# Optimization experiments

Measured on AMD Instinct MI355X. Metric: run time of the kernel, lower is better.

Reference implementation:

```python
import jax, jax.numpy as jnp
import numpy as np

H, DK = 8, 64
INNER = H * DK  # 512


def rel_shift(x):
    # Transformer-XL relative shift (NeMo style): pad left, reshape, drop first row.
    b, h, q, p = x.shape
    x = jnp.pad(x, ((0, 0), (0, 0), (0, 0), (1, 0)))
    x = x.reshape(b, h, p + 1, q)[:, :, 1:]
    return x.reshape(b, h, q, p)


def setup_inputs() -> dict:
    key = jax.random.key(0)
    ks = jax.random.split(key, 16)
    B, T, D = 8, 1024, 512
    s_d = 1.0 / np.sqrt(D)
    s_i = 1.0 / np.sqrt(INNER)
    return {
        "x": jax.random.normal(ks[0], (B, T, D), jnp.float32),
        "pos_emb": jax.random.normal(ks[1], (1, 2 * T - 1, INNER), jnp.float32),
        "w_qkv": jax.random.normal(ks[2], (D, 3 * INNER), jnp.float32) * s_d,
        "w_q": jax.random.normal(ks[3], (INNER, INNER), jnp.float32) * s_i,
        "b_q": jnp.zeros((INNER,), jnp.float32),
        "w_k": jax.random.normal(ks[4], (INNER, INNER), jnp.float32) * s_i,
        "b_k": jnp.zeros((INNER,), jnp.float32),
        "w_v": jax.random.normal(ks[5], (INNER, INNER), jnp.float32) * s_i,
        "b_v": jnp.zeros((INNER,), jnp.float32),
        "w_pos": jax.random.normal(ks[6], (INNER, INNER), jnp.float32) * s_i,
        "bias_u": jax.random.normal(ks[7], (H, DK), jnp.float32) * 0.02,
        "bias_v": jax.random.normal(ks[8], (H, DK), jnp.float32) * 0.02,
        "w_ao": jax.random.normal(ks[9], (INNER, INNER), jnp.float32) * s_i,
        "b_ao": jnp.zeros((INNER,), jnp.float32),
        "w_o": jax.random.normal(ks[10], (INNER, D), jnp.float32) * s_i,
        "b_o": jnp.zeros((D,), jnp.float32),
    }


def reference(x, pos_emb, w_qkv, w_q, b_q, w_k, b_k, w_v, b_v, w_pos,
              bias_u, bias_v, w_ao, b_ao, w_o, b_o):
    B, T, D = x.shape
    # wrapper qkv projection (no bias), then chunk
    q, k, v = jnp.split(x @ w_qkv, 3, axis=-1)
    # RelPositionMultiHeadAttention internal projections
    q = (q @ w_q + b_q).reshape(B, T, H, DK)                       # (b,t,h,d)
    k = (k @ w_k + b_k).reshape(B, T, H, DK).transpose(0, 2, 1, 3)  # (b,h,t,d)
    v = (v @ w_v + b_v).reshape(B, T, H, DK).transpose(0, 2, 1, 3)  # (b,h,t,d)
    p = (pos_emb @ w_pos).reshape(pos_emb.shape[0], -1, H, DK).transpose(0, 2, 1, 3)  # (1,h,2t-1,d)
    q_u = (q + bias_u).transpose(0, 2, 1, 3)  # (b,h,t,d)
    q_v = (q + bias_v).transpose(0, 2, 1, 3)
    matrix_ac = jnp.einsum('bhqd,bhkd->bhqk', q_u, k)      # (b,h,t,t)
    matrix_bd = jnp.einsum('bhqd,xhpd->bhqp', q_v, p)      # (b,h,t,2t-1)
    matrix_bd = rel_shift(matrix_bd)[..., :T]
    scores = (matrix_ac + matrix_bd) * (1.0 / np.sqrt(DK))
    attn = jax.nn.softmax(scores, axis=-1)  # mask=None, dropout inactive at eval
    out = jnp.einsum('bhqk,bhkd->bhqd', attn, v)
    out = out.transpose(0, 2, 1, 3).reshape(B, T, INNER)
    out = out @ w_ao + b_ao   # attention linear_out
    return out @ w_o + b_o    # wrapper to_out
```

## Files before the change

kernel.cpp:

```cpp
#include <hip/hip_runtime.h>
#include <hip/hip_bf16.h>
#include <math.h>

#define H_     8
#define DK_    64
#define INNER_ 512
#define B_     8
#define T_     1024
#define D_     512
#define PLEN_  2047
#define BT_    8192

typedef __attribute__((ext_vector_type(8))) short bf16x8;
typedef __attribute__((ext_vector_type(4))) float f32x4;
typedef __attribute__((ext_vector_type(4))) unsigned short u16x4;
typedef __attribute__((ext_vector_type(8))) unsigned short u16x8;

__device__ __forceinline__ unsigned short f2bf(float f) {
    unsigned u = __float_as_uint(f);
    u += 0x7fffu + ((u >> 16) & 1u);
    return (unsigned short)(u >> 16);
}
__device__ __forceinline__ float bf2f(unsigned short s) {
    return __uint_as_float(((unsigned)s) << 16);
}
__device__ __forceinline__ f32x4 mfma16(bf16x8 a, bf16x8 b, f32x4 c) {
    return __builtin_amdgcn_mfma_f32_16x16x32_bf16(a, b, c, 0, 0, 0);
}
__device__ __forceinline__ void gload16(const unsigned short* g, unsigned short* l) {
    __builtin_amdgcn_global_load_lds(
        (const __attribute__((address_space(1))) void*)g,
        (__attribute__((address_space(3))) void*)l,
        16, 0, 0);
}
#define BARRIER()  __builtin_amdgcn_s_barrier()
#define SCHEDBAR() __builtin_amdgcn_sched_barrier(0)
#define VMCNT(N)   asm volatile("s_waitcnt vmcnt(" #N ")" ::: "memory")

#define QSCALE 0.125f

struct SplitA {
    const float* s[4];
    unsigned short* h[4];
    unsigned short* l[4];
    long n[4];
    int wantl[4];
};
__global__ __launch_bounds__(256) void split4(SplitA a)
{
    const int seg = blockIdx.y;
    long i4 = ((long)blockIdx.x * 256 + threadIdx.x) * 4;
    if (i4 >= a.n[seg]) return;
    f32x4 v = *(const f32x4*)(a.s[seg] + i4);
    u16x4 hh, ll;
    #pragma unroll
    for (int i = 0; i < 4; ++i) {
        unsigned short hb = f2bf(v[i]);
        hh[i] = hb;
        ll[i] = f2bf(v[i] - bf2f(hb));
    }
    *(u16x4*)(a.h[seg] + i4) = hh;
    if (a.wantl[seg]) *(u16x4*)(a.l[seg] + i4) = ll;
}

struct PrepW {
    const float* w[5];
    unsigned short* wh[5];
    unsigned short* wl[5];
};
__global__ __launch_bounds__(256) void prep_wb(PrepW p)
{
    const int z = blockIdx.z;
    const float* w = p.w[z];
    unsigned short* wh = p.wh[z];
    unsigned short* wl = p.wl[z];
    __shared__ float sW[32][36];
    const int t = threadIdx.x;
    const int n0 = blockIdx.x * 32, k0 = blockIdx.y * 32;
    {
        int kr = t >> 3, c4 = (t & 7) * 4;
        f32x4 v = *(const f32x4*)(w + (size_t)(k0 + kr) * 512 + n0 + c4);
        #pragma unroll
        for (int i = 0; i < 4; ++i) sW[kr][c4 + i] = v[i];
    }
    __syncthreads();
    {
        int nr = t >> 3, kc = (t & 7) * 4;
        u16x4 hv, lv;
        #pragma unroll
        for (int i = 0; i < 4; ++i) {
            float f = sW[kc + i][nr];
            unsigned short hb = f2bf(f);
            hv[i] = hb;
            lv[i] = f2bf(f - bf2f(hb));
        }
        *(u16x4*)(wh + (size_t)(n0 + nr) * 512 + k0 + kc) = hv;
        *(u16x4*)(wl + (size_t)(n0 + nr) * 512 + k0 + kc) = lv;
    }
}

__global__ __launch_bounds__(256) void misc_k(
    const float* __restrict__ b_ao, const float* __restrict__ w_o,
    const float* __restrict__ b_o, float* __restrict__ be,
    unsigned short* __restrict__ pb_base)
{
    if (blockIdx.x < 2) {
        int n = blockIdx.x * 256 + threadIdx.x;
        float s = b_o[n];
        for (int j = 0; j < 512; ++j) s += b_ao[j] * w_o[(size_t)j * 512 + n];
        be[n] = s;
    } else {
        ((unsigned int*)pb_base)[threadIdx.x] = 0u;
    }
}

template<int MF, bool ALO>
__device__ __forceinline__ void gemm_core(
    f32x4 (&acc)[MF][4],
    const unsigned short* __restrict__ Ah_g,
    const unsigned short* __restrict__ Al_g, int lda,
    const unsigned short* __restrict__ Wh_g,
    const unsigned short* __restrict__ Wl_g,
    int M, int row0, int col0,
    unsigned short* sAh, unsigned short* sAl,
    unsigned short* sWh, unsigned short* sWl)
{
    const int t = threadIdx.x;
    const int lane = t & 63, w = t >> 6;
    const int wm = w >> 1, wn = w & 1;
    const int ln15 = lane & 15, g4 = lane >> 4;
    const int ASZ = MF * 32 * 32;
    const int WSZ = 128 * 32;
    constexpr int NLD = (MF / 2) * (ALO ? 2 : 1) + 4;

    auto stage = [&](int kt, int buf) {
        #pragma unroll
        for (int l = 0; l < MF / 2; ++l) {
            int e = l * 256 + w * 64 + lane;
            int row = e >> 2, slot = e & 3;
            int ss = slot ^ (row & 3);
            int gr = row0 + row;
            if (gr > M - 1) gr = M - 1;
            size_t ga = (size_t)gr * lda + kt * 32 + ss * 8;
            gload16(Ah_g + ga, sAh + buf * ASZ + (l * 256 + w * 64) * 8);
            if constexpr (ALO)
                gload16(Al_g + ga, sAl + buf * ASZ + (l * 256 + w * 64) * 8);
        }
        #pragma unroll
        for (int l = 0; l < 2; ++l) {
            int e = l * 256 + w * 64 + lane;
            int row = e >> 2, slot = e & 3;
            int ss = slot ^ (row & 3);
            size_t gw = (size_t)(col0 + row) * 512 + kt * 32 + ss * 8;
            gload16(Wh_g + gw, sWh + buf * WSZ + (l * 256 + w * 64) * 8);
            gload16(Wl_g + gw, sWl + buf * WSZ + (l * 256 + w * 64) * 8);
        }
    };
    auto comp = [&](int buf) {
        bf16x8 fah[MF], fal[MF], fwh[4], fwl[4];
        #pragma unroll
        for (int i = 0; i < MF; ++i) {
            int ar = wm * (MF * 16) + i * 16 + ln15;
            int sa = (g4 ^ (ar & 3)) * 8;
            fah[i] = *(const bf16x8*)&sAh[buf * ASZ + ar * 32 + sa];
            if constexpr (ALO)
                fal[i] = *(const bf16x8*)&sAl[buf * ASZ + ar * 32 + sa];
        }
        #pragma unroll
        for (int j = 0; j < 4; ++j) {
            int wr = wn * 64 + j * 16 + ln15;
            int sw = (g4 ^ (wr & 3)) * 8;
            fwh[j] = *(const bf16x8*)&sWh[buf * WSZ + wr * 32 + sw];
            fwl[j] = *(const bf16x8*)&sWl[buf * WSZ + wr * 32 + sw];
        }
        __builtin_amdgcn_s_setprio(1);
        #pragma unroll
        for (int mi = 0; mi < MF; ++mi)
            #pragma unroll
            for (int ni = 0; ni < 4; ++ni) {
                acc[mi][ni] = mfma16(fah[mi], fwh[ni], acc[mi][ni]);
                acc[mi][ni] = mfma16(fah[mi], fwl[ni], acc[mi][ni]);
                if constexpr (ALO)
                    acc[mi][ni] = mfma16(fal[mi], fwh[ni], acc[mi][ni]);
            }
        __builtin_amdgcn_s_setprio(0);
    };

    stage(0, 0);
    for (int k2 = 0; k2 < 8; ++k2) {
        BARRIER();
        stage(2 * k2 + 1, 1);
        if constexpr (NLD == 6) { VMCNT(6); } else { VMCNT(8); }
        BARRIER(); SCHEDBAR();
        comp(0);
        BARRIER();
        if (k2 < 7) {
            stage(2 * k2 + 2, 0);
            if constexpr (NLD == 6) { VMCNT(6); } else { VMCNT(8); }
        } else {
            VMCNT(0);
        }
        BARRIER(); SCHEDBAR();
        comp(1);
    }
}

#define GEMM_LDS3(MF) \
    __shared__ __align__(16) unsigned short sAh[2][MF * 32 * 32]; \
    __shared__ __align__(16) unsigned short sAl[2][MF * 32 * 32]; \
    __shared__ __align__(16) unsigned short sWh[2][128 * 32];     \
    __shared__ __align__(16) unsigned short sWl[2][128 * 32];
#define GEMM_LDS2(MF) \
    __shared__ __align__(16) unsigned short sAh[2][MF * 32 * 32]; \
    __shared__ __align__(16) unsigned short sWh[2][128 * 32];     \
    __shared__ __align__(16) unsigned short sWl[2][128 * 32];

__global__ __launch_bounds__(256, 3) void gemm_qkvp(
    const unsigned short* __restrict__ Ah_g,
    const unsigned short* __restrict__ Wh_g,
    const unsigned short* __restrict__ Wl_g,
    const unsigned short* __restrict__ posh,
    const unsigned short* __restrict__ wp_h,
    const unsigned short* __restrict__ wp_l,
    const float* __restrict__ b_q, const float* __restrict__ bu,
    const float* __restrict__ bv, const float* __restrict__ b_k,
    const float* __restrict__ b_v,
    unsigned short* __restrict__ qu, unsigned short* __restrict__ qv,
    unsigned short* __restrict__ kb, unsigned short* __restrict__ vt,
    unsigned short* __restrict__ pb0)
{
    GEMM_LDS2(4)
    f32x4 acc[4][4];
    #pragma unroll
    for (int i = 0; i < 4; ++i)
        #pragma unroll
        for (int j = 0; j < 4; ++j) acc[i][j] = (f32x4){0.f, 0.f, 0.f, 0.f};

    const int bx = blockIdx.x, by = blockIdx.y;
    const bool isPos = (bx == 12);
    int row0, col0, M;
    const unsigned short *Ag, *Whg, *Wlg;
    if (isPos) {
        row0 = (by >> 2) * 128; col0 = (by & 3) * 128;
        Ag = posh; Whg = wp_h; Wlg = wp_l; M = PLEN_;
    } else {
        row0 = by * 128; col0 = bx * 128;
        Ag = Ah_g; Whg = Wh_g; Wlg = Wl_g; M = BT_;
    }
    gemm_core<4, false>(acc, Ag, nullptr, 512, Whg, Wlg, M, row0, col0,
                        &sAh[0][0], &sAh[0][0], &sWh[0][0], &sWl[0][0]);

    const int t = threadIdx.x;
    const int lane = t & 63, w = t >> 6;
    const int wm = w >> 1, wn = w & 1;
    const int ln15 = lane & 15, g4 = lane >> 4;

    if (isPos) {
        #pragma unroll
        for (int mi = 0; mi < 4; ++mi)
            #pragma unroll
            for (int r4 = 0; r4 < 4; ++r4) {
                int gr = row0 + wm * 64 + mi * 16 + g4 * 4 + r4;
                if (gr >= PLEN_) continue;
                #pragma unroll
                for (int ni = 0; ni < 4; ++ni) {
                    int gc = col0 + wn * 64 + ni * 16 + ln15;
                    pb0[(size_t)gr * 512 + gc] = f2bf(acc[mi][ni][r4]);
                }
            }
        return;
    }

    const int grp = col0 >> 9;
    if (grp == 2) {
        #pragma unroll
        for (int mi = 0; mi < 4; ++mi) {
            int gr0 = row0 + wm * 64 + mi * 16 + g4 * 4;
            int bb = gr0 >> 10, t0 = gr0 & 1023;
            #pragma unroll
            for (int ni = 0; ni < 4; ++ni) {
                int gcl = (col0 & 511) + wn * 64 + ni * 16 + ln15;
                float bias = b_v[gcl];
                u16x4 vv;
                #pragma unroll
                for (int r4 = 0; r4 < 4; ++r4) vv[r4] = f2bf(acc[mi][ni][r4] + bias);
                *(u16x4*)(vt + ((size_t)(bb * 512 + gcl)) * 1024 + t0) = vv;
            }
        }
    } else {
        #pragma unroll
        for (int mi = 0; mi < 4; ++mi)
            #pragma unroll
            for (int r4 = 0; r4 < 4; ++r4) {
                int gr = row0 + wm * 64 + mi * 16 + g4 * 4 + r4;
                #pragma unroll
                for (int ni = 0; ni < 4; ++ni) {
                    int gcl = (col0 & 511) + wn * 64 + ni * 16 + ln15;
                    float a = acc[mi][ni][r4];
                    if (grp == 0) {
                        float base = a + b_q[gcl];
                        qu[(size_t)gr * 512 + gcl] = f2bf((base + bu[gcl]) * QSCALE);
                        qv[(size_t)gr * 512 + gcl] = f2bf((base + bv[gcl]) * QSCALE);
                    } else {
                        kb[(size_t)gr * 512 + gcl] = f2bf(a + b_k[gcl]);
                    }
                }
            }
    }
}

struct WeffA {
    const unsigned short* ah[4];
    const unsigned short* al[4];
    int lda[4];
    const unsigned short* wh[4];
    const unsigned short* wl[4];
    float* c[4];
};
__global__ __launch_bounds__(256, 3) void gemm_weff(WeffA a)
{
    GEMM_LDS3(2)
    const int z = blockIdx.z;
    f32x4 acc[2][4];
    #pragma unroll
    for (int i = 0; i < 2; ++i)
        #pragma unroll
        for (int j = 0; j < 4; ++j) acc[i][j] = (f32x4){0.f, 0.f, 0.f, 0.f};
    const int row0 = blockIdx.y * 64, col0 = blockIdx.x * 128;
    gemm_core<2, true>(acc, a.ah[z], a.al[z], a.lda[z], a.wh[z], a.wl[z],
                       512, row0, col0,
                       &sAh[0][0], &sAl[0][0], &sWh[0][0], &sWl[0][0]);

    const int t = threadIdx.x;
    const int lane = t & 63, w = t >> 6;
    const int wm = w >> 1, wn = w & 1;
    const int ln15 = lane & 15, g4 = lane >> 4;
    float* C = a.c[z];
    #pragma unroll
    for (int mi = 0; mi < 2; ++mi)
        #pragma unroll
        for (int r4 = 0; r4 < 4; ++r4) {
            int gr = row0 + wm * 32 + mi * 16 + g4 * 4 + r4;
            #pragma unroll
            for (int ni = 0; ni < 4; ++ni) {
                int gc = col0 + wn * 64 + ni * 16 + ln15;
                C[(size_t)gr * 512 + gc] = acc[mi][ni][r4];
            }
        }
}

__global__ __launch_bounds__(256, 3) void gemm_out(
    const unsigned short* __restrict__ Ah_g,
    const unsigned short* __restrict__ Al_g,
    const unsigned short* __restrict__ Wh_g,
    const unsigned short* __restrict__ Wl_g,
    const float* __restrict__ beff, float* __restrict__ C)
{
    GEMM_LDS3(2)
    f32x4 acc[2][4];
    #pragma unroll
    for (int i = 0; i < 2; ++i)
        #pragma unroll
        for (int j = 0; j < 4; ++j) acc[i][j] = (f32x4){0.f, 0.f, 0.f, 0.f};
    const int row0 = blockIdx.y * 64, col0 = blockIdx.x * 128;
    gemm_core<2, true>(acc, Ah_g, Al_g, 512, Wh_g, Wl_g, BT_, row0, col0,
                       &sAh[0][0], &sAl[0][0], &sWh[0][0], &sWl[0][0]);

    const int t = threadIdx.x;
    const int lane = t & 63, w = t >> 6;
    const int wm = w >> 1, wn = w & 1;
    const int ln15 = lane & 15, g4 = lane >> 4;
    #pragma unroll
    for (int mi = 0; mi < 2; ++mi)
        #pragma unroll
        for (int r4 = 0; r4 < 4; ++r4) {
            int gr = row0 + wm * 32 + mi * 16 + g4 * 4 + r4;
            #pragma unroll
            for (int ni = 0; ni < 4; ++ni) {
                int gc = col0 + wn * 64 + ni * 16 + ln15;
                C[(size_t)gr * 512 + gc] = acc[mi][ni][r4] + beff[gc];
            }
        }
}

__global__ __launch_bounds__(256, 2) void attn_v12(
    const unsigned short* __restrict__ qu_g,
    const unsigned short* __restrict__ qv_g,
    const unsigned short* __restrict__ kb_g,
    const unsigned short* __restrict__ vt_g,
    const unsigned short* __restrict__ pb_g,
    unsigned short* __restrict__ atth,
    unsigned short* __restrict__ attl)
{
    __shared__ __align__(16) unsigned short sK[2][64 * 64];
    __shared__ __align__(16) unsigned short sP[2][64 * 64];
    __shared__ __align__(16) unsigned short sV[2][64 * 64];
    __shared__ __align__(16) unsigned short ringb[64][132];
    __shared__ __align__(16) unsigned short sProb[64][72];

    const int t = threadIdx.x;
    const int lane = t & 63, w = t >> 6;
    const int ln15 = lane & 15, g4 = lane >> 4;

    const int wg = blockIdx.x;
    const int idx = (wg & 7) * 128 + (wg >> 3);
    const int q0 = (idx & 15) * 64;
    const int bh = idx >> 4;
    const int h = bh & 7, b = bh >> 3;
    const size_t tok0 = (size_t)b * T_;
    const int hd = h * DK_;
    const int qq = w * 16 + ln15;

    auto stage_chunk = [&](int c, int buf) {
        #pragma unroll
        for (int l = 0; l < 2; ++l) {
            int e = l * 256 + w * 64 + lane;
            int row = e >> 3, slot = e & 7;
            int sl = slot ^ (row & 7);
            int lofs = buf * 4096 + (l * 256 + w * 64) * 8;
            gload16(kb_g + (tok0 + c * 64 + row) * INNER_ + hd + sl * 8, &sK[0][lofs]);
            gload16(vt_g + ((size_t)(b * H_ + h) * DK_ + row) * T_ + c * 64 + sl * 8, &sV[0][lofs]);
            long p = (long)(c * 64 - q0 + 1023 + row);
            gload16(pb_g + p * INNER_ + hd + sl * 8, &sP[0][lofs]);
        }
    };

    #pragma unroll
    for (int l = 0; l < 2; ++l) {
        int e = l * 256 + w * 64 + lane;
        int row = e >> 3, slot = e & 7;
        int sl = slot ^ (row & 7);
        size_t src = (tok0 + q0 + row) * INNER_ + hd + sl * 8;
        gload16(qu_g + src, &sK[0][(l * 256 + w * 64) * 8]);
        gload16(qv_g + src, &sP[0][(l * 256 + w * 64) * 8]);
    }
    __syncthreads();
    bf16x8 fqu[2], fqv[2];
    #pragma unroll
    for (int ki = 0; ki < 2; ++ki) {
        int sl = (ki * 4 + g4) ^ (qq & 7);
        fqu[ki] = *(const bf16x8*)&sK[0][qq * 64 + sl * 8];
        fqv[ki] = *(const bf16x8*)&sP[0][qq * 64 + sl * 8];
    }
    __syncthreads();

    #pragma unroll
    for (int l = 0; l < 2; ++l) {
        int e = l * 256 + w * 64 + lane;
        int row = e >> 3, slot = e & 7;
        int sl = slot ^ (row & 7);
        long p = (long)(959 - q0 + row);
        gload16(pb_g + p * INNER_ + hd + sl * 8, &sP[0][4096 + (l * 256 + w * 64) * 8]);
    }
    stage_chunk(0, 0);
    __syncthreads();

    #pragma unroll
    for (int n = 0; n < 4; ++n) {
        f32x4 bdv = {0.f, 0.f, 0.f, 0.f};
        #pragma unroll
        for (int ki = 0; ki < 2; ++ki) {
            int prow = n * 16 + ln15;
            int sl = (ki * 4 + g4) ^ (prow & 7);
            bf16x8 pf = *(const bf16x8*)&sP[0][4096 + prow * 64 + sl * 8];
            bdv = mfma16(pf, fqv[ki], bdv);
        }
        #pragma unroll
        for (int r4 = 0; r4 < 4; ++r4)
            ringb[qq][(n * 16 + g4 * 4 + r4 + qq) & 127] = f2bf(bdv[r4]);
    }
    __syncthreads();

    float m = -1e30f, den = 0.f;
    f32x4 o[4];
    #pragma unroll
    for (int i = 0; i < 4; ++i) o[i] = (f32x4){0.f, 0.f, 0.f, 0.f};

    auto compute_chunk = [&](int c, int buf) {
        const int bofs = buf * 4096;
        f32x4 sc[4], bd[4];
        #pragma unroll
        for (int n = 0; n < 4; ++n) {
            sc[n] = (f32x4){0.f, 0.f, 0.f, 0.f};
            bd[n] = (f32x4){0.f, 0.f, 0.f, 0.f};
        }
        __builtin_amdgcn_s_setprio(1);
        #pragma unroll
        for (int ki = 0; ki < 2; ++ki)
            #pragma unroll
            for (int n = 0; n < 4; ++n) {
                int krow = n * 16 + ln15;
                int sl = (ki * 4 + g4) ^ (krow & 7);
                bf16x8 kf = *(const bf16x8*)&sK[0][bofs + krow * 64 + sl * 8];
                sc[n] = mfma16(kf, fqu[ki], sc[n]);
                bf16x8 pf = *(const bf16x8*)&sP[0][bofs + krow * 64 + sl * 8];
                bd[n] = mfma16(pf, fqv[ki], bd[n]);
            }
        __builtin_amdgcn_s_setprio(0);

        const int pbase = (c & 1) ? 0 : 64;
        #pragma unroll
        for (int n = 0; n < 4; ++n)
            #pragma unroll
            for (int r4 = 0; r4 < 4; ++r4)
                ringb[qq][(pbase + n * 16 + g4 * 4 + r4 + qq) & 127] = f2bf(bd[n][r4]);

        float s[4][4];
        float mx = -1e30f;
        #pragma unroll
        for (int n = 0; n < 4; ++n) {
            const int st2 = (c * 64 + 64 + n * 16 + g4 * 4) & 127;
            u16x4 rv = *(const u16x4*)&ringb[qq][st2];
            #pragma unroll
            for (int r4 = 0; r4 < 4; ++r4) {
                float v = sc[n][r4] + bf2f(rv[r4]);
                s[n][r4] = v;
                mx = fmaxf(mx, v);
            }
        }
        mx = fmaxf(mx, __shfl_xor(mx, 16));
        mx = fmaxf(mx, __shfl_xor(mx, 32));
        float newm = fmaxf(m, mx);
        float scale = __expf(m - newm);
        m = newm;
        float ls = 0.f;
        #pragma unroll
        for (int n = 0; n < 4; ++n) {
            u16x4 pv4;
            #pragma unroll
            for (int r4 = 0; r4 < 4; ++r4) {
                float p = __expf(s[n][r4] - newm);
                ls += p;
                pv4[r4] = f2bf(p);
            }
            *(u16x4*)&sProb[qq][n * 16 + g4 * 4] = pv4;
        }
        ls += __shfl_xor(ls, 16);
        ls += __shfl_xor(ls, 32);
        den = den * scale + ls;
        #pragma unroll
        for (int n2 = 0; n2 < 4; ++n2) {
            o[n2][0] *= scale; o[n2][1] *= scale;
            o[n2][2] *= scale; o[n2][3] *= scale;
        }

        __builtin_amdgcn_s_setprio(1);
        #pragma unroll
        for (int ki = 0; ki < 2; ++ki) {
            bf16x8 pa = *(const bf16x8*)&sProb[qq][ki * 32 + g4 * 8];
            #pragma unroll
            for (int n2 = 0; n2 < 4; ++n2) {
                int drow = n2 * 16 + ln15;
                int sl = (ki * 4 + g4) ^ (drow & 7);
                bf16x8 vf = *(const bf16x8*)&sV[0][bofs + drow * 64 + sl * 8];
                o[n2] = mfma16(vf, pa, o[n2]);
            }
        }
        __builtin_amdgcn_s_setprio(0);
    };

    for (int c2 = 0; c2 < 8; ++c2) {
        int c = c2 * 2;
        stage_chunk(c + 1, 1);
        compute_chunk(c, 0);
        __syncthreads();
        if (c2 < 7) stage_chunk(c + 2, 0);
        compute_chunk(c + 1, 1);
        __syncthreads();
    }

    const float inv = 1.0f / den;
    #pragma unroll
    for (int n2 = 0; n2 < 4; ++n2) {
        u16x4 hv, lv;
        #pragma unroll
        for (int r4 = 0; r4 < 4; ++r4) {
            float val = o[n2][r4] * inv;
            unsigned short hb = f2bf(val);
            hv[r4] = hb;
            lv[r4] = f2bf(val - bf2f(hb));
        }
        size_t oidx = (tok0 + q0 + qq) * INNER_ + hd + n2 * 16 + g4 * 4;
        *(u16x4*)(atth + oidx) = hv;
        *(u16x4*)(attl + oidx) = lv;
    }
}

extern "C" void kernel_launch(void* const* d_in, const int* in_sizes, int n_in,
                              void* d_out, int out_size, void* d_ws, size_t ws_size,
                              hipStream_t stream)
{
    const float* x     = (const float*)d_in[0];
    const float* pos   = (const float*)d_in[1];
    const float* w_qkv = (const float*)d_in[2];
    const float* w_q   = (const float*)d_in[3];
    const float* b_q   = (const float*)d_in[4];
    const float* w_k   = (const float*)d_in[5];
    const float* b_k   = (const float*)d_in[6];
    const float* w_v   = (const float*)d_in[7];
    const float* b_v   = (const float*)d_in[8];
    const float* w_pos = (const float*)d_in[9];
    const float* bu    = (const float*)d_in[10];
    const float* bv    = (const float*)d_in[11];
    const float* w_ao  = (const float*)d_in[12];
    const float* b_ao  = (const float*)d_in[13];
    const float* w_o   = (const float*)d_in[14];
    const float* b_o   = (const float*)d_in[15];
    float* out = (float*)d_out;

    unsigned short* u = (unsigned short*)d_ws;
    const size_t SZ = (size_t)BT_ * INNER_;
    unsigned short* xh   = u;
    unsigned short* xl   = xh + SZ;
    unsigned short* qu   = xl + SZ;
    unsigned short* qv   = qu + SZ;
    unsigned short* kb   = qv + SZ;
    unsigned short* vt   = kb + SZ;
    unsigned short* atth = vt + SZ;
    unsigned short* attl = atth + SZ;
    unsigned short* pb_base = attl + SZ;
    unsigned short* pb0  = pb_base + 512;
    unsigned short* posh = pb_base + 1049600;
    unsigned short* posl = posh + 1049600;
    unsigned short* wqkvh = posl + 1049600;
    unsigned short* wqkvl = wqkvh + 786432;
    unsigned short* waoh  = wqkvl + 786432;
    unsigned short* waol  = waoh + 262144;
    unsigned short* w5    = waol + 262144;
    unsigned short* wq_h = w5;              unsigned short* wq_l = w5 + 262144;
    unsigned short* wk_h = w5 + 2*262144;   unsigned short* wk_l = w5 + 3*262144;
    unsigned short* wv_h = w5 + 4*262144;   unsigned short* wv_l = w5 + 5*262144;
    unsigned short* wo_h = w5 + 6*262144;   unsigned short* wo_l = w5 + 7*262144;
    unsigned short* wp_h = w5 + 8*262144;   unsigned short* wp_l = w5 + 9*262144;
    float* weffC = (float*)(w5 + 10*262144);
    unsigned short* wcat_h = (unsigned short*)(weffC + 4*262144);
    unsigned short* wcat_l = wcat_h + 786432;
    unsigned short* woe_h  = wcat_l + 786432;
    unsigned short* woe_l  = woe_h + 262144;
    float* beff = (float*)(woe_l + 262144);

    dim3 blk(256);

    SplitA sa;
    sa.s[0] = x;     sa.h[0] = xh;    sa.l[0] = xl;    sa.n[0] = (long)SZ;          sa.wantl[0] = 0;
    sa.s[1] = w_qkv; sa.h[1] = wqkvh; sa.l[1] = wqkvl; sa.n[1] = 786432L;           sa.wantl[1] = 1;
    sa.s[2] = w_ao;  sa.h[2] = waoh;  sa.l[2] = waol;  sa.n[2] = 262144L;           sa.wantl[2] = 1;
    sa.s[3] = pos;   sa.h[3] = posh;  sa.l[3] = posl;  sa.n[3] = (long)PLEN_ * 512; sa.wantl[3] = 0;
    split4<<<dim3(4096, 4), blk, 0, stream>>>(sa);

    PrepW p5;
    p5.w[0] = w_q;   p5.wh[0] = wq_h; p5.wl[0] = wq_l;
    p5.w[1] = w_k;   p5.wh[1] = wk_h; p5.wl[1] = wk_l;
    p5.w[2] = w_v;   p5.wh[2] = wv_h; p5.wl[2] = wv_l;
    p5.w[3] = w_o;   p5.wh[3] = wo_h; p5.wl[3] = wo_l;
    p5.w[4] = w_pos; p5.wh[4] = wp_h; p5.wl[4] = wp_l;
    prep_wb<<<dim3(16, 16, 5), blk, 0, stream>>>(p5);

    WeffA wa;
    wa.ah[0] = wqkvh;        wa.al[0] = wqkvl;        wa.lda[0] = 1536;
    wa.ah[1] = wqkvh + 512;  wa.al[1] = wqkvl + 512;  wa.lda[1] = 1536;
    wa.ah[2] = wqkvh + 1024; wa.al[2] = wqkvl + 1024; wa.lda[2] = 1536;
    wa.ah[3] = waoh;         wa.al[3] = waol;         wa.lda[3] = 512;
    wa.wh[0] = wq_h; wa.wl[0] = wq_l;
    wa.wh[1] = wk_h; wa.wl[1] = wk_l;
    wa.wh[2] = wv_h; wa.wl[2] = wv_l;
    wa.wh[3] = wo_h; wa.wl[3] = wo_l;
    wa.c[0] = weffC;             wa.c[1] = weffC + 262144;
    wa.c[2] = weffC + 2*262144;  wa.c[3] = weffC + 3*262144;
    gemm_weff<<<dim3(4, 8, 4), blk, 0, stream>>>(wa);

    PrepW p4;
    p4.w[0] = weffC;            p4.wh[0] = wcat_h;            p4.wl[0] = wcat_l;
    p4.w[1] = weffC + 262144;   p4.wh[1] = wcat_h + 262144;   p4.wl[1] = wcat_l + 262144;
    p4.w[2] = weffC + 2*262144; p4.wh[2] = wcat_h + 2*262144; p4.wl[2] = wcat_l + 2*262144;
    p4.w[3] = weffC + 3*262144; p4.wh[3] = woe_h;             p4.wl[3] = woe_l;
    p4.w[4] = nullptr; p4.wh[4] = nullptr; p4.wl[4] = nullptr;
    prep_wb<<<dim3(16, 16, 4), blk, 0, stream>>>(p4);

    misc_k<<<3, blk, 0, stream>>>(b_ao, w_o, b_o, beff, pb_base);

    gemm_qkvp<<<dim3(13, 64), blk, 0, stream>>>(xh, wcat_h, wcat_l,
        posh, wp_h, wp_l,
        b_q, bu, bv, b_k, b_v, qu, qv, kb, vt, pb0);

    attn_v12<<<1024, blk, 0, stream>>>(qu, qv, kb, vt, pb0, atth, attl);

    gemm_out<<<dim3(4, 128), blk, 0, stream>>>(atth, attl, woe_h, woe_l, beff, out);
}
```

Measured before the change: 188.3 us.

## Single-buffer attention K/P/V tiles to raise occupancy to three blocks per CU

Shrinks the shared K, P and V staging from double buffers to single buffers and changes the loop to load, sync, compute, sync for each chunk. Launch bounds go from 2 to 3 blocks per CU, so more workgroups can hide latency across blocks instead of prefetching within one. The cost is that global loads are no longer overlapped with compute inside a block, and the tighter register limit may cause spills.

```diff
diff --git a/kernel.cpp b/kernel.cpp
--- a/kernel.cpp
+++ b/kernel.cpp
@@ -383,7 +383,7 @@
         }
 }
 
-__global__ __launch_bounds__(256, 2) void attn_v12(
+__global__ __launch_bounds__(256, 3) void attn_v13(
     const unsigned short* __restrict__ qu_g,
     const unsigned short* __restrict__ qv_g,
     const unsigned short* __restrict__ kb_g,
@@ -392,9 +392,9 @@
     unsigned short* __restrict__ atth,
     unsigned short* __restrict__ attl)
 {
-    __shared__ __align__(16) unsigned short sK[2][64 * 64];
-    __shared__ __align__(16) unsigned short sP[2][64 * 64];
-    __shared__ __align__(16) unsigned short sV[2][64 * 64];
+    __shared__ __align__(16) unsigned short sK[64 * 64];
+    __shared__ __align__(16) unsigned short sP[64 * 64];
+    __shared__ __align__(16) unsigned short sV[64 * 64];
     __shared__ __align__(16) unsigned short ringb[64][132];
     __shared__ __align__(16) unsigned short sProb[64][72];
 
@@ -411,17 +411,17 @@
     const int hd = h * DK_;
     const int qq = w * 16 + ln15;
 
-    auto stage_chunk = [&](int c, int buf) {
+    auto stage_chunk = [&](int c) {
         #pragma unroll
         for (int l = 0; l < 2; ++l) {
             int e = l * 256 + w * 64 + lane;
             int row = e >> 3, slot = e & 7;
             int sl = slot ^ (row & 7);
-            int lofs = buf * 4096 + (l * 256 + w * 64) * 8;
-            gload16(kb_g + (tok0 + c * 64 + row) * INNER_ + hd + sl * 8, &sK[0][lofs]);
-            gload16(vt_g + ((size_t)(b * H_ + h) * DK_ + row) * T_ + c * 64 + sl * 8, &sV[0][lofs]);
+            int lofs = (l * 256 + w * 64) * 8;
+            gload16(kb_g + (tok0 + c * 64 + row) * INNER_ + hd + sl * 8, &sK[lofs]);
+            gload16(vt_g + ((size_t)(b * H_ + h) * DK_ + row) * T_ + c * 64 + sl * 8, &sV[lofs]);
             long p = (long)(c * 64 - q0 + 1023 + row);
-            gload16(pb_g + p * INNER_ + hd + sl * 8, &sP[0][lofs]);
+            gload16(pb_g + p * INNER_ + hd + sl * 8, &sP[lofs]);
         }
     };
 
@@ -431,16 +431,16 @@
         int row = e >> 3, slot = e & 7;
         int sl = slot ^ (row & 7);
         size_t src = (tok0 + q0 + row) * INNER_ + hd + sl * 8;
-        gload16(qu_g + src, &sK[0][(l * 256 + w * 64) * 8]);
-        gload16(qv_g + src, &sP[0][(l * 256 + w * 64) * 8]);
+        gload16(qu_g + src, &sK[(l * 256 + w * 64) * 8]);
+        gload16(qv_g + src, &sP[(l * 256 + w * 64) * 8]);
     }
     __syncthreads();
     bf16x8 fqu[2], fqv[2];
     #pragma unroll
     for (int ki = 0; ki < 2; ++ki) {
         int sl = (ki * 4 + g4) ^ (qq & 7);
-        fqu[ki] = *(const bf16x8*)&sK[0][qq * 64 + sl * 8];
-        fqv[ki] = *(const bf16x8*)&sP[0][qq * 64 + sl * 8];
+        fqu[ki] = *(const bf16x8*)&sK[qq * 64 + sl * 8];
+        fqv[ki] = *(const bf16x8*)&sP[qq * 64 + sl * 8];
     }
     __syncthreads();
 
@@ -450,9 +450,8 @@
         int row = e >> 3, slot = e & 7;
         int sl = slot ^ (row & 7);
         long p = (long)(959 - q0 + row);
-        gload16(pb_g + p * INNER_ + hd + sl * 8, &sP[0][4096 + (l * 256 + w * 64) * 8]);
-    }
-    stage_chunk(0, 0);
+        gload16(pb_g + p * INNER_ + hd + sl * 8, &sP[(l * 256 + w * 64) * 8]);
+    }
     __syncthreads();
 
     #pragma unroll
@@ -462,7 +461,7 @@
         for (int ki = 0; ki < 2; ++ki) {
             int prow = n * 16 + ln15;
             int sl = (ki * 4 + g4) ^ (prow & 7);
-            bf16x8 pf = *(const bf16x8*)&sP[0][4096 + prow * 64 + sl * 8];
+            bf16x8 pf = *(const bf16x8*)&sP[prow * 64 + sl * 8];
             bdv = mfma16(pf, fqv[ki], bdv);
         }
         #pragma unroll
@@ -476,8 +475,7 @@
     #pragma unroll
     for (int i = 0; i < 4; ++i) o[i] = (f32x4){0.f, 0.f, 0.f, 0.f};
 
-    auto compute_chunk = [&](int c, int buf) {
-        const int bofs = buf * 4096;
+    auto compute_chunk = [&](int c) {
         f32x4 sc[4], bd[4];
         #pragma unroll
         for (int n = 0; n < 4; ++n) {
@@ -491,9 +489,9 @@
             for (int n = 0; n < 4; ++n) {
                 int krow = n * 16 + ln15;
                 int sl = (ki * 4 + g4) ^ (krow & 7);
-                bf16x8 kf = *(const bf16x8*)&sK[0][bofs + krow * 64 + sl * 8];
+                bf16x8 kf = *(const bf16x8*)&sK[krow * 64 + sl * 8];
                 sc[n] = mfma16(kf, fqu[ki], sc[n]);
-                bf16x8 pf = *(const bf16x8*)&sP[0][bofs + krow * 64 + sl * 8];
+                bf16x8 pf = *(const bf16x8*)&sP[krow * 64 + sl * 8];
                 bd[n] = mfma16(pf, fqv[ki], bd[n]);
             }
         __builtin_amdgcn_s_setprio(0);
@@ -552,20 +550,17 @@
             for (int n2 = 0; n2 < 4; ++n2) {
                 int drow = n2 * 16 + ln15;
                 int sl = (ki * 4 + g4) ^ (drow & 7);
-                bf16x8 vf = *(const bf16x8*)&sV[0][bofs + drow * 64 + sl * 8];
+                bf16x8 vf = *(const bf16x8*)&sV[drow * 64 + sl * 8];
                 o[n2] = mfma16(vf, pa, o[n2]);
             }
         }
         __builtin_amdgcn_s_setprio(0);
     };
 
-    for (int c2 = 0; c2 < 8; ++c2) {
-        int c = c2 * 2;
-        stage_chunk(c + 1, 1);
-        compute_chunk(c, 0);
+    for (int c = 0; c < 16; ++c) {
+        stage_chunk(c);
         __syncthreads();
-        if (c2 < 7) stage_chunk(c + 2, 0);
-        compute_chunk(c + 1, 1);
+        compute_chunk(c);
         __syncthreads();
     }
 
@@ -683,7 +678,7 @@
         posh, wp_h, wp_l,
         b_q, bu, bv, b_k, b_v, qu, qv, kb, vt, pb0);
 
-    attn_v12<<<1024, blk, 0, stream>>>(qu, qv, kb, vt, pb0, atth, attl);
+    attn_v13<<<1024, blk, 0, stream>>>(qu, qv, kb, vt, pb0, atth, attl);
 
     gemm_out<<<dim3(4, 128), blk, 0, stream>>>(atth, attl, woe_h, woe_l, beff, out);
 }
```

After: 190.6 us. About the same (+1.2%).
